# Kernel tuning notes

Measured on AMD Instinct MI355X. Metric: run time of the kernel, lower is better.

The kernel has to match this reference:

```python
import jax, jax.numpy as jnp
import numpy as np

KSIZE = 9
D_IN_HALF = 256   # channels after GLU
D_MODEL = 512     # conv output / LSTM hidden size


def setup_inputs() -> dict:
    key = jax.random.key(0)
    ks = jax.random.split(key, 8)
    s = 1.0 / np.sqrt(D_MODEL)
    return {
        "x": jax.random.normal(ks[0], (16, 512, 512), dtype=jnp.float32),
        # Conv1d(256->512, kernel_size=1) == pointwise linear
        "conv_w": jax.random.normal(ks[1], (D_MODEL, D_IN_HALF), dtype=jnp.float32) * (1.0 / np.sqrt(D_IN_HALF)),
        "conv_b": jax.random.normal(ks[2], (D_MODEL,), dtype=jnp.float32) * 0.01,
        # LSTM(512, 512), torch gate order: i, f, g, o
        "w_ih": jax.random.normal(ks[3], (4 * D_MODEL, D_MODEL), dtype=jnp.float32) * s,
        "w_hh": jax.random.normal(ks[4], (4 * D_MODEL, D_MODEL), dtype=jnp.float32) * s,
        "b_ih": jax.random.normal(ks[5], (4 * D_MODEL,), dtype=jnp.float32) * s,
        "b_hh": jax.random.normal(ks[6], (4 * D_MODEL,), dtype=jnp.float32) * s,
    }


def _lstm_last_hidden(seq, w_ih, w_hh, b_ih, b_hh):
    # seq: [N, K, D] -> last hidden state [N, D]
    N, K, D = seq.shape
    h0 = jnp.zeros((N, D), seq.dtype)
    c0 = jnp.zeros((N, D), seq.dtype)

    def step(carry, xt):
        h, c = carry
        gates = xt @ w_ih.T + b_ih + h @ w_hh.T + b_hh  # [N, 4D]
        i, f, g, o = jnp.split(gates, 4, axis=-1)
        c = jax.nn.sigmoid(f) * c + jax.nn.sigmoid(i) * jnp.tanh(g)
        h = jax.nn.sigmoid(o) * jnp.tanh(c)
        return (h, c), None

    (h, _), _ = jax.lax.scan(step, (h0, c0), jnp.swapaxes(seq, 0, 1))
    return h


def reference(x, conv_w, conv_b, w_ih, w_hh, b_ih, b_hh):
    # GLU over last dim: a * sigmoid(b)
    a, b = jnp.split(x, 2, axis=-1)
    x = a * jax.nn.sigmoid(b)                       # [B, L, 256]
    # Conv1d kernel_size=1 == pointwise linear
    x = jnp.einsum('blc,dc->bld', x, conv_w) + conv_b  # [B, L, 512]
    B, L, D = x.shape
    K = KSIZE
    # get_K: left-pad K-1 zeros, gather overlapping windows
    xp = jnp.concatenate([jnp.zeros((B, K - 1, D), x.dtype), x], axis=1)
    idx = jnp.arange(L)[:, None] + jnp.arange(K)[None, :]  # [L, K]
    win = xp[:, idx]                                # [B, L, K, D]
    h = _lstm_last_hidden(win.reshape(B * L, K, D), w_ih, w_hh, b_ih, b_hh)
    return h.reshape(B, L, D)
```

## Files before the change

### kernel.cpp

```cpp
#include <hip/hip_runtime.h>
#include <stdint.h>

using half8 = __attribute__((ext_vector_type(8))) _Float16;
using half4 = __attribute__((ext_vector_type(4))) _Float16;
using f32x4 = __attribute__((ext_vector_type(4))) float;

#define OFF_XPROJT 0ULL
#define OFF_WHH    34078720ULL
#define OFF_WCF    36175872ULL
#define OFF_BC     37224448ULL
#define OFF_B0     37232640ULL

__device__ __forceinline__ float sigm(float x){ return 1.0f/(1.0f + __expf(-x)); }
__device__ __forceinline__ float tanh_(float x){ float e = __expf(2.0f*x); return 1.0f - 2.0f/(e + 1.0f); }

__global__ void prep1(const float* __restrict__ conv_w, const float* __restrict__ conv_b,
                      const float* __restrict__ w_ih, const float* __restrict__ b_ih,
                      const float* __restrict__ b_hh, float* __restrict__ Wc,
                      float* __restrict__ bc_perm, float* __restrict__ b0_perm){
  int bid = blockIdx.x, t = threadIdx.x;
  if (bid < 1024) {
    int r0 = bid*2;
    float a0 = 0.f, a1 = 0.f;
    const float* w0 = w_ih + (size_t)r0*512;
    for (int d=0; d<512; ++d){
      float cw = conv_w[d*256 + t];
      a0 = fmaf(w0[d],     cw, a0);
      a1 = fmaf(w0[512+d], cw, a1);
    }
    Wc[(size_t)r0*256 + t]     = a0;
    Wc[(size_t)(r0+1)*256 + t] = a1;
  } else {
    int r = (bid-1024)*256 + t;
    float s = 0.f;
    for (int d=0; d<512; ++d) s = fmaf(w_ih[(size_t)r*512+d], conv_b[d], s);
    int gate = r >> 9, u = r & 511;
    int newc = ((u>>4)<<6) + (gate<<4) + (u&15);
    float bbv = b_ih[r] + b_hh[r];
    b0_perm[newc] = bbv;
    bc_perm[newc] = s + bbv;
  }
}

__global__ void prep2(const float* __restrict__ w_hh, const float* __restrict__ Wc,
                      _Float16* __restrict__ whh_f, _Float16* __restrict__ wc_f){
  int e = blockIdx.x*256 + threadIdx.x;
  if (e < (1<<20)) {
    int j = e&7, lane = (e>>3)&63, t = (e>>9)&127, s = e>>16;
    int newc = t*16 + (lane&15);
    int k = s*32 + (lane>>4)*8 + j;
    int r = (((newc>>4)&3)<<9) + ((newc>>6)<<4) + (newc&15);
    whh_f[e] = (_Float16)w_hh[r*512 + k];
  } else {
    int e2 = e - (1<<20);
    int j = e2&7, lane = (e2>>3)&63, t = (e2>>9)&127, s = e2>>16;
    int newc = t*16 + (lane&15);
    int k = s*32 + (lane>>4)*8 + j;
    int r = (((newc>>4)&3)<<9) + ((newc>>6)<<4) + (newc&15);
    wc_f[e2] = (_Float16)Wc[r*256 + k];
  }
}

__global__ void prefill(const float* __restrict__ b0_perm, _Float16* __restrict__ xprojT){
  int e = blockIdx.x*256 + threadIdx.x;
  int col = e>>7, b = (e>>3)&15, p = e&7;
  xprojT[(size_t)col*8320 + b*520 + p] = (_Float16)b0_perm[col];
}

__global__ __launch_bounds__(512, 2) void xp_kernel(const float* __restrict__ x,
      const _Float16* __restrict__ wc_f, const float* __restrict__ bc_perm,
      _Float16* __restrict__ xprojT){
  __shared__ _Float16 A[32*264];
  int wg = blockIdx.x, tid = threadIdx.x;
  int n0 = wg*32;
  int wv = tid>>6, lane = tid&63, lrow = lane>>4, lcol = lane&15;
  #pragma unroll
  for (int i=0;i<4;++i){
    int q = tid + i*512;
    int row = q>>6, pos = q&63;
    const float* xr = x + (size_t)(n0+row)*512;
    f32x4 va = __builtin_nontemporal_load((const f32x4*)(xr + pos*4));
    f32x4 vb = __builtin_nontemporal_load((const f32x4*)(xr + 256 + pos*4));
    half4 h;
    h[0] = (_Float16)(va[0] / (1.f+__expf(-vb[0])));
    h[1] = (_Float16)(va[1] / (1.f+__expf(-vb[1])));
    h[2] = (_Float16)(va[2] / (1.f+__expf(-vb[2])));
    h[3] = (_Float16)(va[3] / (1.f+__expf(-vb[3])));
    *(half4*)&A[row*264 + pos*4] = h;
  }
  f32x4 acc[2][16];
  #pragma unroll
  for (int nt=0;nt<16;++nt){
    int col = (wv*16+nt)*16 + lcol;
    float b = bc_perm[col];
    f32x4 v = {b,b,b,b};
    acc[0][nt]=v; acc[1][nt]=v;
  }
  __syncthreads();
  for (int s=0;s<8;++s){
    half8 a0 = *(const half8*)&A[lcol*264 + s*32 + lrow*8];
    half8 a1 = *(const half8*)&A[(16+lcol)*264 + s*32 + lrow*8];
    #pragma unroll
    for (int nt=0;nt<16;++nt){
      int t = wv*16+nt;
      half8 b = *(const half8*)(wc_f + ((s*128 + t)*64 + lane)*8);
      acc[0][nt] = __builtin_amdgcn_mfma_f32_16x16x32_f16(a0, b, acc[0][nt], 0,0,0);
      acc[1][nt] = __builtin_amdgcn_mfma_f32_16x16x32_f16(a1, b, acc[1][nt], 0,0,0);
    }
  }
  #pragma unroll
  for (int m=0;m<2;++m)
    #pragma unroll
    for (int nt=0;nt<16;++nt){
      int col = (wv*16+nt)*16 + lcol;
      int n = n0 + m*16 + lrow*4;
      half4 hv;
      hv[0]=(_Float16)acc[m][nt][0]; hv[1]=(_Float16)acc[m][nt][1];
      hv[2]=(_Float16)acc[m][nt][2]; hv[3]=(_Float16)acc[m][nt][3];
      *(half4*)&xprojT[(size_t)col*8320 + (size_t)(n>>9)*520 + 8 + (n&511)] = hv;
    }
}


#define ISSUE4(SP, GQ, BUF) { \
  const char* gp = whhB + ((((size_t)(SP))*128 + tb + (GQ)*4) << 10) + (lane<<4); \
  char* lpb = (char*)&CHUNK[wv][BUF][0]; \
  _Pragma("unroll") for (int jj=0;jj<4;++jj) \
    __builtin_amdgcn_global_load_lds((const __attribute__((address_space(1))) void*)(gp + (jj<<10)), \
        (__attribute__((address_space(3))) void*)(lpb + (jj<<10)), 16, 0, 0); }

#define GMFMA(G_) \
    _Pragma("unroll") for (int j=0;j<4;++j){ \
      half8 bf = *(const half8*)&CHUNK[wv][(G_)&1][j*1024 + lane*16]; \
      acc[0][(G_)*4+j] = __builtin_amdgcn_mfma_f32_16x16x32_f16(a0, bf, acc[0][(G_)*4+j],0,0,0); \
      acc[1][(G_)*4+j] = __builtin_amdgcn_mfma_f32_16x16x32_f16(a1, bf, acc[1][(G_)*4+j],0,0,0); }

#define GBODY_ISSUE(S_, G_) { \
    ISSUE4(((G_)<3 ? (S_) : (S_)+1), (((G_)+1)&3), (((G_)+1)&1)); \
    asm volatile("s_waitcnt vmcnt(4)" ::: "memory"); \
    __builtin_amdgcn_sched_barrier(0); \
    GMFMA(G_) }

#define GBODY_LAST(G_) { \
    asm volatile("s_waitcnt vmcnt(0)" ::: "memory"); \
    __builtin_amdgcn_sched_barrier(0); \
    GMFMA(G_) }

__global__ __launch_bounds__(512, 2) void lstm_kernel(const _Float16* __restrict__ xprojT,
      const _Float16* __restrict__ whh_f, float* __restrict__ out){
  __shared__ _Float16 H[32*520];
  __shared__ __attribute__((aligned(16))) char CHUNK[8][2][4096];
  int wg = blockIdx.x, tid = threadIdx.x;
  int n0 = wg*32, l0 = n0 & 511, bb = n0 >> 9;
  int wv = tid>>6, lane = tid&63, lrow = lane>>4, lcol = lane&15;
  int tb = wv*16;
  const char* whhB = (const char*)whh_f;

  f32x4 c[2][4];
  #pragma unroll
  for (int m=0;m<2;++m)
    #pragma unroll
    for (int g=0;g<4;++g) c[m][g] = (f32x4){0.f,0.f,0.f,0.f};

  #pragma unroll 1
  for (int k=0;k<9;++k){
    f32x4 acc[2][16];
    {
      int sh = (k&1)*16;
      size_t segb = (size_t)bb*520 + l0 + k;
      #pragma unroll
      for (int m=0;m<2;++m)
        #pragma unroll
        for (int nt=0;nt<16;++nt){
          size_t S = (size_t)((tb+nt)*16 + lcol)*8320 + segb + m*16 + lrow*4;
          const uint32_t* p = (const uint32_t*)(xprojT + (S & ~(size_t)1));
          uint32_t d0 = p[0], d1 = p[1], d2 = p[2];
          uint32_t lo = __builtin_amdgcn_alignbit(d1, d0, sh);
          uint32_t hi = __builtin_amdgcn_alignbit(d2, d1, sh);
          union { uint32_t u; _Float16 h[2]; } ua, ub;
          ua.u = lo; ub.u = hi;
          acc[m][nt] = (f32x4){(float)ua.h[0], (float)ua.h[1], (float)ub.h[0], (float)ub.h[1]};
        }
    }
    __builtin_amdgcn_sched_barrier(0);
    if (k > 0){
      ISSUE4(0, 0, 0);
      #pragma unroll 1
      for (int s=0;s<15;++s){
        half8 a0 = *(const half8*)&H[lcol*520 + s*32 + lrow*8];
        half8 a1 = *(const half8*)&H[(16+lcol)*520 + s*32 + lrow*8];
        GBODY_ISSUE(s,0) GBODY_ISSUE(s,1) GBODY_ISSUE(s,2) GBODY_ISSUE(s,3)
      }
      {
        half8 a0 = *(const half8*)&H[lcol*520 + 15*32 + lrow*8];
        half8 a1 = *(const half8*)&H[(16+lcol)*520 + 15*32 + lrow*8];
        GBODY_ISSUE(15,0) GBODY_ISSUE(15,1) GBODY_ISSUE(15,2) GBODY_LAST(3)
      }
    }
    __syncthreads();
    #pragma unroll
    for (int m=0;m<2;++m)
      #pragma unroll
      for (int ub=0;ub<4;++ub){
        f32x4 gi = acc[m][ub*4+0], gf = acc[m][ub*4+1];
        f32x4 gg = acc[m][ub*4+2], go = acc[m][ub*4+3];
        #pragma unroll
        for (int reg=0;reg<4;++reg){
          float cn = sigm(gf[reg])*c[m][ub][reg] + sigm(gi[reg])*tanh_(gg[reg]);
          c[m][ub][reg] = cn;
          float h = sigm(go[reg])*tanh_(cn);
          int row = m*16 + lrow*4 + reg;
          int u = (wv*4+ub)*16 + lcol;
          if (k < 8) H[row*520 + u] = (_Float16)h;
          else __builtin_nontemporal_store(h, &out[(size_t)(n0+row)*512 + u]);
        }
      }
    __syncthreads();
  }
}

extern "C" void kernel_launch(void* const* d_in, const int* in_sizes, int n_in,
                              void* d_out, int out_size, void* d_ws, size_t ws_size,
                              hipStream_t stream){
  const float* x      = (const float*)d_in[0];
  const float* conv_w = (const float*)d_in[1];
  const float* conv_b = (const float*)d_in[2];
  const float* w_ih   = (const float*)d_in[3];
  const float* w_hh   = (const float*)d_in[4];
  const float* b_ih   = (const float*)d_in[5];
  const float* b_hh   = (const float*)d_in[6];
  char* ws = (char*)d_ws;
  _Float16* xprojT = (_Float16*)(ws + OFF_XPROJT);
  _Float16* whh_f  = (_Float16*)(ws + OFF_WHH);
  _Float16* wc_f   = (_Float16*)(ws + OFF_WCF);
  float* Wc        = (float*)(ws + 0);
  float* bc_perm   = (float*)(ws + OFF_BC);
  float* b0_perm   = (float*)(ws + OFF_B0);
  float* out = (float*)d_out;

  prep1<<<1032, 256, 0, stream>>>(conv_w, conv_b, w_ih, b_ih, b_hh, Wc, bc_perm, b0_perm);
  prep2<<<6144, 256, 0, stream>>>(w_hh, Wc, whh_f, wc_f);
  prefill<<<1024, 256, 0, stream>>>(b0_perm, xprojT);
  xp_kernel<<<256, 512, 0, stream>>>(x, wc_f, bc_perm, xprojT);
  lstm_kernel<<<256, 512, 0, stream>>>(xprojT, whh_f, out);
}
```

Before: 565.1 us.

## Overlap input-projection loads with recurrent MFMA loop via in-loop prefetch

Replaces the up-front gather of the precomputed input projection before each LSTM step with prefetches spread through the fully unrolled recurrent GEMM loop. Accumulators start at zero and the prefetched fp16 projection values are added after each group of rows, so global-load latency hides behind MFMA work instead of stalling the step start. The s-loop is now fully unrolled and vmcnt waits are adjusted to account for the extra outstanding loads. This costs code size and register pressure from the prefetch buffers under a 2-blocks-per-CU launch bound.

New measurement: 1.557 ms. 175% more time.

```diff
diff --git a/kernel.cpp b/kernel.cpp
--- a/kernel.cpp
+++ b/kernel.cpp
@@ -4,6 +4,7 @@
 using half8 = __attribute__((ext_vector_type(8))) _Float16;
 using half4 = __attribute__((ext_vector_type(4))) _Float16;
 using f32x4 = __attribute__((ext_vector_type(4))) float;
+typedef uint32_t u32x3 __attribute__((ext_vector_type(3), aligned(4)));
 
 #define OFF_XPROJT 0ULL
 #define OFF_WHH    34078720ULL
@@ -122,29 +123,63 @@
 }
 
 
+#define STRX(x) #x
+#define WAITC(N) { asm volatile("s_waitcnt vmcnt(" STRX(N) ")" ::: "memory"); \
+                   __builtin_amdgcn_sched_barrier(0); }
+
 #define ISSUE4(SP, GQ, BUF) { \
-  const char* gp = whhB + ((((size_t)(SP))*128 + tb + (GQ)*4) << 10) + (lane<<4); \
-  char* lpb = (char*)&CHUNK[wv][BUF][0]; \
+  const char* gp_ = whhB + ((((size_t)(SP))*128 + tb + (GQ)*4) << 10) + (lane<<4); \
+  char* lpb_ = (char*)&CHUNK[wv][BUF][0]; \
   _Pragma("unroll") for (int jj=0;jj<4;++jj) \
-    __builtin_amdgcn_global_load_lds((const __attribute__((address_space(1))) void*)(gp + (jj<<10)), \
-        (__attribute__((address_space(3))) void*)(lpb + (jj<<10)), 16, 0, 0); }
-
-#define GMFMA(G_) \
+    __builtin_amdgcn_global_load_lds((const __attribute__((address_space(1))) void*)(gp_ + (jj<<10)), \
+        (__attribute__((address_space(3))) void*)(lpb_ + (jj<<10)), 16, 0, 0); }
+
+#define GMFMA(G_) { \
     _Pragma("unroll") for (int j=0;j<4;++j){ \
       half8 bf = *(const half8*)&CHUNK[wv][(G_)&1][j*1024 + lane*16]; \
       acc[0][(G_)*4+j] = __builtin_amdgcn_mfma_f32_16x16x32_f16(a0, bf, acc[0][(G_)*4+j],0,0,0); \
-      acc[1][(G_)*4+j] = __builtin_amdgcn_mfma_f32_16x16x32_f16(a1, bf, acc[1][(G_)*4+j],0,0,0); }
+      acc[1][(G_)*4+j] = __builtin_amdgcn_mfma_f32_16x16x32_f16(a1, bf, acc[1][(G_)*4+j],0,0,0); } }
+
+#define PF8(PG) { \
+  _Pragma("unroll") for (int jn=0;jn<4;++jn){ \
+    _Pragma("unroll") for (int m=0;m<2;++m){ \
+      pf[jn*2+m] = *(const u32x3*)(ak + (size_t)((PG)*4+jn)*266240 + m*32); } } }
+
+#define CVTADD(PG) { \
+  _Pragma("unroll") for (int jn=0;jn<4;++jn){ \
+    _Pragma("unroll") for (int m=0;m<2;++m){ \
+      u32x3 v_ = pf[jn*2+m]; \
+      uint32_t lo_ = __builtin_amdgcn_alignbit(v_[1], v_[0], sh); \
+      uint32_t hi_ = __builtin_amdgcn_alignbit(v_[2], v_[1], sh); \
+      union { uint32_t u; _Float16 h[2]; } ua_, ub_; ua_.u = lo_; ub_.u = hi_; \
+      f32x4 g_ = {(float)ua_.h[0],(float)ua_.h[1],(float)ub_.h[0],(float)ub_.h[1]}; \
+      acc[m][(PG)*4+jn] += g_; } } }
 
 #define GBODY_ISSUE(S_, G_) { \
     ISSUE4(((G_)<3 ? (S_) : (S_)+1), (((G_)+1)&3), (((G_)+1)&1)); \
-    asm volatile("s_waitcnt vmcnt(4)" ::: "memory"); \
+    WAITC(4) GMFMA(G_) }
+
+#define GBODY_W8(S_, G_) { \
+    ISSUE4(((G_)<3 ? (S_) : (S_)+1), (((G_)+1)&3), (((G_)+1)&1)); \
+    WAITC(8) GMFMA(G_) }
+
+#define GBODY_PF(S_, G_, PG) { \
+    ISSUE4(((G_)<3 ? (S_) : (S_)+1), (((G_)+1)&3), (((G_)+1)&1)); \
     __builtin_amdgcn_sched_barrier(0); \
-    GMFMA(G_) }
-
-#define GBODY_LAST(G_) { \
-    asm volatile("s_waitcnt vmcnt(0)" ::: "memory"); \
-    __builtin_amdgcn_sched_barrier(0); \
-    GMFMA(G_) }
+    PF8(PG) \
+    WAITC(8) GMFMA(G_) }
+
+#define GBODY_LAST(G_) { WAITC(0) GMFMA(G_) }
+
+#define AFRAGS(S_) \
+    half8 a0 = *(const half8*)&H[lcol*520 + (S_)*32 + lrow*8]; \
+    half8 a1 = *(const half8*)&H[(16+lcol)*520 + (S_)*32 + lrow*8];
+
+#define ROWA(S_) { AFRAGS(S_) \
+    GBODY_ISSUE(S_,0) GBODY_ISSUE(S_,1) GBODY_ISSUE(S_,2) GBODY_ISSUE(S_,3) }
+
+#define ROWPF(S_, PG) { AFRAGS(S_) \
+    GBODY_PF(S_,0,PG) GBODY_W8(S_,1) GBODY_ISSUE(S_,2) GBODY_ISSUE(S_,3) }
 
 __global__ __launch_bounds__(512, 2) void lstm_kernel(const _Float16* __restrict__ xprojT,
       const _Float16* __restrict__ whh_f, float* __restrict__ out){
@@ -155,47 +190,42 @@
   int wv = tid>>6, lane = tid&63, lrow = lane>>4, lcol = lane&15;
   int tb = wv*16;
   const char* whhB = (const char*)whh_f;
+  const char* gbase = (const char*)xprojT
+      + (size_t)(tb*16 + lcol)*16640 + (size_t)bb*1040 + (size_t)l0*2 + (size_t)lrow*8;
 
   f32x4 c[2][4];
   #pragma unroll
   for (int m=0;m<2;++m)
     #pragma unroll
     for (int g=0;g<4;++g) c[m][g] = (f32x4){0.f,0.f,0.f,0.f};
+
+  u32x3 pf[8];
 
   #pragma unroll 1
   for (int k=0;k<9;++k){
     f32x4 acc[2][16];
-    {
-      int sh = (k&1)*16;
-      size_t segb = (size_t)bb*520 + l0 + k;
+    #pragma unroll
+    for (int m=0;m<2;++m)
       #pragma unroll
-      for (int m=0;m<2;++m)
-        #pragma unroll
-        for (int nt=0;nt<16;++nt){
-          size_t S = (size_t)((tb+nt)*16 + lcol)*8320 + segb + m*16 + lrow*4;
-          const uint32_t* p = (const uint32_t*)(xprojT + (S & ~(size_t)1));
-          uint32_t d0 = p[0], d1 = p[1], d2 = p[2];
-          uint32_t lo = __builtin_amdgcn_alignbit(d1, d0, sh);
-          uint32_t hi = __builtin_amdgcn_alignbit(d2, d1, sh);
-          union { uint32_t u; _Float16 h[2]; } ua, ub;
-          ua.u = lo; ub.u = hi;
-          acc[m][nt] = (f32x4){(float)ua.h[0], (float)ua.h[1], (float)ub.h[0], (float)ub.h[1]};
-        }
-    }
-    __builtin_amdgcn_sched_barrier(0);
+      for (int nt=0;nt<16;++nt) acc[m][nt] = (f32x4){0.f,0.f,0.f,0.f};
+    const char* ak = gbase + (size_t)(2*k - 2*(k&1));
+    unsigned sh = (unsigned)((k&1)*16);
+
     if (k > 0){
       ISSUE4(0, 0, 0);
-      #pragma unroll 1
-      for (int s=0;s<15;++s){
-        half8 a0 = *(const half8*)&H[lcol*520 + s*32 + lrow*8];
-        half8 a1 = *(const half8*)&H[(16+lcol)*520 + s*32 + lrow*8];
-        GBODY_ISSUE(s,0) GBODY_ISSUE(s,1) GBODY_ISSUE(s,2) GBODY_ISSUE(s,3)
-      }
-      {
-        half8 a0 = *(const half8*)&H[lcol*520 + 15*32 + lrow*8];
-        half8 a1 = *(const half8*)&H[(16+lcol)*520 + 15*32 + lrow*8];
-        GBODY_ISSUE(15,0) GBODY_ISSUE(15,1) GBODY_ISSUE(15,2) GBODY_LAST(3)
-      }
+      __builtin_amdgcn_sched_barrier(0);
+      ROWA(0) ROWA(1) ROWA(2) ROWPF(3,0)
+      CVTADD(0)
+      ROWA(4) ROWA(5) ROWA(6) ROWPF(7,1)
+      CVTADD(1)
+      ROWA(8) ROWA(9) ROWA(10) ROWPF(11,2)
+      CVTADD(2)
+      ROWA(12) ROWA(13) ROWA(14)
+      { AFRAGS(15)
+        GBODY_PF(15,0,3) GBODY_W8(15,1) GBODY_ISSUE(15,2) GBODY_LAST(3) }
+      CVTADD(3)
+    } else {
+      PF8(0) CVTADD(0) PF8(1) CVTADD(1) PF8(2) CVTADD(2) PF8(3) CVTADD(3)
     }
     __syncthreads();
     #pragma unroll
```
